# Performance work log

Measured on AMD Instinct MI355X. Metric: run time of the kernel, lower is better.

## Reference

```python
import jax, jax.numpy as jnp
import numpy as np


def conv1d_same(x, w, b, dilation=1):
    # x: [B, T, Cin], w: [K, Cin, Cout] (WIO), 'same' padding, stride 1
    y = jax.lax.conv_general_dilated(
        x, w, window_strides=(1,), padding='SAME',
        rhs_dilation=(dilation,), dimension_numbers=('NWC', 'WIO', 'NWC'))
    return y + b


def setup_inputs() -> dict:
    key = jax.random.key(0)
    ks = jax.random.split(key, 6)
    B, T, N_IN, N_OUT, ATTN_DIM, KSZ = 16, 2048, 96, 128, 64, 3
    return {
        'x': jax.random.normal(ks[0], (B, T, N_IN), jnp.float32),
        'qkv_w': jax.random.normal(ks[1], (N_IN, 3 * ATTN_DIM), jnp.float32) * 0.05,
        'qkv_b': jnp.zeros((3 * ATTN_DIM,), jnp.float32),
        'scale': jnp.ones((), jnp.float32),
        'conv_w1': jax.random.normal(ks[2], (KSZ, ATTN_DIM, N_OUT), jnp.float32) * 0.05,
        'conv_b1': jnp.zeros((N_OUT,), jnp.float32),
        'conv_w2': jax.random.normal(ks[3], (KSZ, N_OUT, N_OUT), jnp.float32) * 0.05,
        'conv_b2': jnp.zeros((N_OUT,), jnp.float32),
        'down_w': jax.random.normal(ks[4], (N_IN, N_OUT), jnp.float32) * 0.1,
    }


def reference(x, qkv_w, qkv_b, scale, conv_w1, conv_b1, conv_w2, conv_b2, down_w):
    # Dense4Attention: single Dense(3*attn_dim), split into q,k,v
    qkv = x @ qkv_w + qkv_b                       # [B,T,3*D]
    q, k, v = jnp.split(qkv, 3, axis=-1)          # each [B,T,D]
    # AttentionBlock: scores = q k^T * learned scale; non-causal (default)
    scores = jnp.einsum('btd,bsd->bts', q, k) * scale   # [B,T,T]
    weights = jax.nn.softmax(scores, axis=2)            # softmax_axis=2
    out_attn = jnp.einsum('bts,bsd->btd', weights, v)   # [B,T,D]
    h = jax.nn.relu(conv1d_same(out_attn, conv_w1, conv_b1, 1))
    out = jax.nn.relu(conv1d_same(h, conv_w2, conv_b2, 1))   # [B,T,n_out]
    # enhanced residual: softmax over time of row-sums of attn weights
    weight_x = jax.nn.softmax(jnp.sum(weights, axis=2), axis=1)  # [B,T]
    en_res_x = (weight_x[..., None] * x) @ down_w   # n_in != n_out -> downsample
    res = x @ down_w                                 # skip path downsample
    return jax.nn.relu(out + res + en_res_x)
```

## Files before the change

kernel.cpp:

```cpp
#include <hip/hip_runtime.h>
#include <cstdint>

#define B_   16
#define T_   2048
#define CIN  96
#define DH   64
#define NOUT 128

typedef float floatx4 __attribute__((ext_vector_type(4)));
typedef short shortx8 __attribute__((ext_vector_type(8)));

__device__ __forceinline__ unsigned short f2bf(float f) {
  unsigned int u = __float_as_uint(f);
  u += 0x7FFFu + ((u >> 16) & 1u);
  return (unsigned short)(u >> 16);
}
__device__ __forceinline__ floatx4 f4zero() { floatx4 v; v[0]=0.f;v[1]=0.f;v[2]=0.f;v[3]=0.f; return v; }
__device__ __forceinline__ shortx8 s8zero() { shortx8 v;
#pragma unroll
  for (int i=0;i<8;++i) v[i]=0; return v; }

__global__ __launch_bounds__(256) void k_wprep(
    const float* __restrict__ qkv_w, const float* __restrict__ cw1,
    const float* __restrict__ cw2, const float* __restrict__ dw,
    unsigned short* __restrict__ qwt, unsigned short* __restrict__ w1t,
    unsigned short* __restrict__ w2t, unsigned short* __restrict__ dwt)
{
  int o = blockIdx.x * 256 + threadIdx.x;
  if (o < 18432) {
    int co = o / 96, ci = o % 96;
    qwt[o] = f2bf(qkv_w[ci * 192 + co]);
  } else if (o < 43008) {
    int p = o - 18432;
    int tap = p / 8192, rem = p % 8192, co = rem >> 6, ci = rem & 63;
    w1t[p] = f2bf(cw1[(tap * 64 + ci) * 128 + co]);
  } else if (o < 92160) {
    int p = o - 43008;
    int tap = p / 16384, rem = p % 16384, co = rem >> 7, ci = rem & 127;
    w2t[p] = f2bf(cw2[(tap * 128 + ci) * 128 + co]);
  } else if (o < 104448) {
    int p = o - 92160;
    int co = p / 96, ci = p % 96;
    dwt[p] = f2bf(dw[ci * 128 + co]);
  }
}

__global__ __launch_bounds__(256) void k_qkv(
    const float* __restrict__ x, const unsigned short* __restrict__ qwt,
    const float* __restrict__ qkv_b, const float* __restrict__ scale_p,
    unsigned short* __restrict__ qb, unsigned short* __restrict__ kb,
    unsigned short* __restrict__ vT)
{
  __shared__ __align__(16) unsigned short Xs[64][104];
  const int bx = blockIdx.x;
  const int b = bx >> 5, t0 = (bx & 31) * 64;
  const int tid = threadIdx.x, wave = tid >> 6, lane = tid & 63;
  const int l15 = lane & 15, quad = lane >> 4;
  const float scl2 = scale_p[0] * 1.4426950408889634f;

  for (int idx = tid; idx < 64 * 24; idx += 256) {
    int r = idx / 24, c = (idx % 24) * 4;
    float4 xv = *(const float4*)(x + ((size_t)(b * T_ + t0 + r)) * CIN + c);
    ushort4 o; o.x = f2bf(xv.x); o.y = f2bf(xv.y); o.z = f2bf(xv.z); o.w = f2bf(xv.w);
    *(ushort4*)(&Xs[r][c]) = o;
  }
  __syncthreads();

  floatx4 acc[4][3];
#pragma unroll
  for (int mt = 0; mt < 4; ++mt)
#pragma unroll
    for (int nt = 0; nt < 3; ++nt) acc[mt][nt] = f4zero();

#pragma unroll
  for (int ks = 0; ks < 3; ++ks) {
    shortx8 wf[3];
#pragma unroll
    for (int nt = 0; nt < 3; ++nt) {
      int j = wave * 48 + nt * 16 + l15;
      wf[nt] = *(const shortx8*)(qwt + (size_t)j * 96 + ks * 32 + quad * 8);
    }
#pragma unroll
    for (int mt = 0; mt < 4; ++mt) {
      shortx8 af = *(const shortx8*)(&Xs[mt * 16 + l15][ks * 32 + quad * 8]);
#pragma unroll
      for (int nt = 0; nt < 3; ++nt)
        acc[mt][nt] = __builtin_amdgcn_mfma_f32_16x16x32_bf16(af, wf[nt], acc[mt][nt], 0, 0, 0);
    }
  }

#pragma unroll
  for (int nt = 0; nt < 3; ++nt) {
    int j0 = wave * 48 + nt * 16;
    int j = j0 + l15;
    float bias = qkv_b[j];
#pragma unroll
    for (int mt = 0; mt < 4; ++mt) {
#pragma unroll
      for (int r = 0; r < 4; ++r) {
        int t = t0 + mt * 16 + quad * 4 + r;
        float v = acc[mt][nt][r] + bias;
        if (j0 < 64)        qb[((size_t)b * T_ + t) * DH + j] = f2bf(v * scl2);
        else if (j0 < 128)  kb[((size_t)b * T_ + t) * DH + (j - 64)] = f2bf(v);
        else                vT[((size_t)b * DH + (j - 128)) * T_ + t] = f2bf(v);
      }
    }
  }
}

__global__ __launch_bounds__(256) void k_attn(
    const unsigned short* __restrict__ qb, const unsigned short* __restrict__ kb,
    const unsigned short* __restrict__ vT,
    float* __restrict__ opart, float* __restrict__ lws)
{
  __shared__ __align__(16) unsigned short Kt[64][72];
  __shared__ __align__(16) unsigned short Vt[80][72];
  __shared__ __align__(16) unsigned short Pt[4][16][72];
  const int bx = blockIdx.x;
  const int half = bx & 1, qt = (bx >> 1) & 31, b = bx >> 6;
  const int tid = threadIdx.x, wave = tid >> 6, lane = tid & 63;
  const int l15 = lane & 15, quad = lane >> 4;

  const unsigned short* qrow = qb + ((size_t)b * T_ + qt * 64 + wave * 16 + l15) * DH;
  shortx8 qf0 = *(const shortx8*)(qrow + quad * 8);
  shortx8 qf1 = *(const shortx8*)(qrow + 32 + quad * 8);

  floatx4 O[5];
#pragma unroll
  for (int i = 0; i < 5; ++i) O[i] = f4zero();

  const unsigned short* kbase = kb + (size_t)b * T_ * DH + (size_t)half * 1024 * DH;
  const unsigned short* vbase = vT + (size_t)b * DH * T_ + half * 1024;

  for (int idx = tid; idx < 16 * 72; idx += 256) {
    int r = idx / 72, c = idx % 72;
    Vt[64 + r][c] = (r == 0) ? (unsigned short)0x3F80 : (unsigned short)0;
  }

  const int kr0 = tid >> 3, kc = (tid & 7) * 8;
  shortx8 pk[2], pv[2];
#pragma unroll
  for (int i = 0; i < 2; ++i) {
    pk[i] = *(const shortx8*)(kbase + (size_t)(kr0 + i * 32) * DH + kc);
    pv[i] = *(const shortx8*)(vbase + (size_t)(kr0 + i * 32) * T_ + kc);
  }

  for (int t = 0; t < 16; ++t) {
#pragma unroll
    for (int i = 0; i < 2; ++i) {
      *(shortx8*)(&Kt[kr0 + i * 32][kc]) = pk[i];
      *(shortx8*)(&Vt[kr0 + i * 32][kc]) = pv[i];
    }
    __syncthreads();

    if (t < 15) {
      int s0 = (t + 1) * 64;
#pragma unroll
      for (int i = 0; i < 2; ++i) {
        pk[i] = *(const shortx8*)(kbase + (size_t)(s0 + kr0 + i * 32) * DH + kc);
        pv[i] = *(const shortx8*)(vbase + (size_t)(kr0 + i * 32) * T_ + s0 + kc);
      }
    }

    floatx4 S[4];
#pragma unroll
    for (int nt = 0; nt < 4; ++nt) {
      S[nt] = f4zero();
      shortx8 bk0 = *(const shortx8*)(&Kt[nt * 16 + l15][quad * 8]);
      shortx8 bk1 = *(const shortx8*)(&Kt[nt * 16 + l15][32 + quad * 8]);
      S[nt] = __builtin_amdgcn_mfma_f32_16x16x32_bf16(qf0, bk0, S[nt], 0, 0, 0);
      S[nt] = __builtin_amdgcn_mfma_f32_16x16x32_bf16(qf1, bk1, S[nt], 0, 0, 0);
    }

#pragma unroll
    for (int r = 0; r < 4; ++r)
#pragma unroll
      for (int nt = 0; nt < 4; ++nt) {
        float p = exp2f(S[nt][r]);
        Pt[wave][quad * 4 + r][(nt * 16 + l15 + (quad << 4)) & 63] = f2bf(p);
      }

#pragma unroll
    for (int kk = 0; kk < 2; ++kk) {
      int pcol = (kk * 32 + quad * 8 + ((l15 >> 2) << 4)) & 63;
      shortx8 ap = *(const shortx8*)(&Pt[wave][l15][pcol]);
#pragma unroll
      for (int dt = 0; dt < 5; ++dt) {
        shortx8 bv = *(const shortx8*)(&Vt[dt * 16 + l15][kk * 32 + quad * 8]);
        O[dt] = __builtin_amdgcn_mfma_f32_16x16x32_bf16(ap, bv, O[dt], 0, 0, 0);
      }
    }
    __syncthreads();
  }

  float* obase = opart + (((size_t)(half * B_ + b) * T_) + qt * 64 + wave * 16) * DH;
#pragma unroll
  for (int r = 0; r < 4; ++r) {
    int row = quad * 4 + r;
#pragma unroll
    for (int dt = 0; dt < 4; ++dt)
      obase[(size_t)row * DH + dt * 16 + l15] = O[dt][r];
    if (l15 == 0)
      lws[half * (B_ * T_) + b * T_ + qt * 64 + wave * 16 + row] = O[4][r];
  }
}

__global__ __launch_bounds__(256) void k_comb(
    const float* __restrict__ opart, const float* __restrict__ lws,
    unsigned short* __restrict__ ab)
{
  int g = blockIdx.x * 256 + threadIdx.x;
  int bt = g >> 4, dg = (g & 15) * 4;
  const size_t HS = (size_t)B_ * T_ * DH;
  float4 p0 = *(const float4*)(opart + (size_t)bt * DH + dg);
  float4 p1 = *(const float4*)(opart + HS + (size_t)bt * DH + dg);
  float inv = 1.f / (lws[bt] + lws[B_ * T_ + bt]);
  ushort4 o;
  o.x = f2bf((p0.x + p1.x) * inv);
  o.y = f2bf((p0.y + p1.y) * inv);
  o.z = f2bf((p0.z + p1.z) * inv);
  o.w = f2bf((p0.w + p1.w) * inv);
  *(ushort4*)(ab + (size_t)bt * DH + dg) = o;
}

__global__ __launch_bounds__(256) void k_conv1(
    const unsigned short* __restrict__ ab, const unsigned short* __restrict__ w1t,
    const float* __restrict__ b1, unsigned short* __restrict__ hb)
{
  __shared__ __align__(16) unsigned short At[66][72];
  const int bx = blockIdx.x;
  const int b = bx >> 5, t0 = (bx & 31) * 64;
  const int tid = threadIdx.x, wave = tid >> 6, lane = tid & 63;
  const int l15 = lane & 15, quad = lane >> 4;

  for (int idx = tid; idx < 66 * 8; idx += 256) {
    int r = idx >> 3, c = (idx & 7) * 8;
    int t = t0 + r - 1;
    shortx8 v = s8zero();
    if (t >= 0 && t < T_) v = *(const shortx8*)(ab + ((size_t)b * T_ + t) * DH + c);
    *(shortx8*)(&At[r][c]) = v;
  }
  __syncthreads();

  floatx4 acc[4][2];
#pragma unroll
  for (int mt = 0; mt < 4; ++mt) { acc[mt][0] = f4zero(); acc[mt][1] = f4zero(); }

#pragma unroll
  for (int tap = 0; tap < 3; ++tap) {
#pragma unroll
    for (int ks = 0; ks < 2; ++ks) {
      shortx8 wf[2];
#pragma unroll
      for (int ct = 0; ct < 2; ++ct) {
        int co = wave * 32 + ct * 16 + l15;
        wf[ct] = *(const shortx8*)(w1t + ((size_t)tap * 128 + co) * 64 + ks * 32 + quad * 8);
      }
#pragma unroll
      for (int mt = 0; mt < 4; ++mt) {
        shortx8 af = *(const shortx8*)(&At[mt * 16 + l15 + tap][ks * 32 + quad * 8]);
        acc[mt][0] = __builtin_amdgcn_mfma_f32_16x16x32_bf16(af, wf[0], acc[mt][0], 0, 0, 0);
        acc[mt][1] = __builtin_amdgcn_mfma_f32_16x16x32_bf16(af, wf[1], acc[mt][1], 0, 0, 0);
      }
    }
  }

#pragma unroll
  for (int ct = 0; ct < 2; ++ct) {
    int co = wave * 32 + ct * 16 + l15;
    float bias = b1[co];
#pragma unroll
    for (int mt = 0; mt < 4; ++mt)
#pragma unroll
      for (int r = 0; r < 4; ++r) {
        int t = t0 + mt * 16 + quad * 4 + r;
        hb[((size_t)b * T_ + t) * NOUT + co] = f2bf(fmaxf(acc[mt][ct][r] + bias, 0.f));
      }
  }
}

__global__ __launch_bounds__(256) void k_conv2(
    const unsigned short* __restrict__ hb, const float* __restrict__ x,
    const unsigned short* __restrict__ w2t, const unsigned short* __restrict__ dwt,
    const float* __restrict__ b2, float* __restrict__ out)
{
  __shared__ __align__(16) unsigned short Ht[66][136];
  __shared__ __align__(16) unsigned short Xt[64][104];
  const int bx = blockIdx.x;
  const int b = bx >> 5, t0 = (bx & 31) * 64;
  const int tid = threadIdx.x, wave = tid >> 6, lane = tid & 63;
  const int l15 = lane & 15, quad = lane >> 4;

  for (int idx = tid; idx < 66 * 16; idx += 256) {
    int r = idx >> 4, c = (idx & 15) * 8;
    int t = t0 + r - 1;
    shortx8 v = s8zero();
    if (t >= 0 && t < T_) v = *(const shortx8*)(hb + ((size_t)b * T_ + t) * NOUT + c);
    *(shortx8*)(&Ht[r][c]) = v;
  }
  for (int idx = tid; idx < 64 * 24; idx += 256) {
    int r = idx / 24, c = (idx % 24) * 4;
    float4 xv = *(const float4*)(x + ((size_t)(b * T_ + t0 + r)) * CIN + c);
    ushort4 o; o.x = f2bf(xv.x); o.y = f2bf(xv.y); o.z = f2bf(xv.z); o.w = f2bf(xv.w);
    *(ushort4*)(&Xt[r][c]) = o;
  }
  __syncthreads();

  floatx4 a2[4][2], ar[4][2];
#pragma unroll
  for (int mt = 0; mt < 4; ++mt) { a2[mt][0]=f4zero(); a2[mt][1]=f4zero(); ar[mt][0]=f4zero(); ar[mt][1]=f4zero(); }

#pragma unroll
  for (int tap = 0; tap < 3; ++tap) {
#pragma unroll
    for (int ks = 0; ks < 4; ++ks) {
      shortx8 wf[2];
#pragma unroll
      for (int ct = 0; ct < 2; ++ct) {
        int co = wave * 32 + ct * 16 + l15;
        wf[ct] = *(const shortx8*)(w2t + ((size_t)tap * 128 + co) * 128 + ks * 32 + quad * 8);
      }
#pragma unroll
      for (int mt = 0; mt < 4; ++mt) {
        shortx8 af = *(const shortx8*)(&Ht[mt * 16 + l15 + tap][ks * 32 + quad * 8]);
        a2[mt][0] = __builtin_amdgcn_mfma_f32_16x16x32_bf16(af, wf[0], a2[mt][0], 0, 0, 0);
        a2[mt][1] = __builtin_amdgcn_mfma_f32_16x16x32_bf16(af, wf[1], a2[mt][1], 0, 0, 0);
      }
    }
  }
#pragma unroll
  for (int ks = 0; ks < 3; ++ks) {
    shortx8 wf[2];
#pragma unroll
    for (int ct = 0; ct < 2; ++ct) {
      int co = wave * 32 + ct * 16 + l15;
      wf[ct] = *(const shortx8*)(dwt + (size_t)co * 96 + ks * 32 + quad * 8);
    }
#pragma unroll
    for (int mt = 0; mt < 4; ++mt) {
      shortx8 af = *(const shortx8*)(&Xt[mt * 16 + l15][ks * 32 + quad * 8]);
      ar[mt][0] = __builtin_amdgcn_mfma_f32_16x16x32_bf16(af, wf[0], ar[mt][0], 0, 0, 0);
      ar[mt][1] = __builtin_amdgcn_mfma_f32_16x16x32_bf16(af, wf[1], ar[mt][1], 0, 0, 0);
    }
  }

  const float kres = 1.0f + 1.0f / 2048.0f;
#pragma unroll
  for (int ct = 0; ct < 2; ++ct) {
    int co = wave * 32 + ct * 16 + l15;
    float bias = b2[co];
#pragma unroll
    for (int mt = 0; mt < 4; ++mt)
#pragma unroll
      for (int r = 0; r < 4; ++r) {
        int t = t0 + mt * 16 + quad * 4 + r;
        float o2 = fmaxf(a2[mt][ct][r] + bias, 0.f);
        out[((size_t)b * T_ + t) * NOUT + co] = fmaxf(o2 + ar[mt][ct][r] * kres, 0.f);
      }
  }
}

extern "C" void kernel_launch(void* const* d_in, const int* in_sizes, int n_in,
                              void* d_out, int out_size, void* d_ws, size_t ws_size,
                              hipStream_t stream) {
  const float* x      = (const float*)d_in[0];
  const float* qkv_w  = (const float*)d_in[1];
  const float* qkv_b  = (const float*)d_in[2];
  const float* scale  = (const float*)d_in[3];
  const float* cw1    = (const float*)d_in[4];
  const float* cb1    = (const float*)d_in[5];
  const float* cw2    = (const float*)d_in[6];
  const float* cb2    = (const float*)d_in[7];
  const float* dw     = (const float*)d_in[8];

  char* ws = (char*)d_ws;
  unsigned short* qb  = (unsigned short*)(ws + 0);
  unsigned short* kb  = (unsigned short*)(ws + 4194304);
  unsigned short* vT  = (unsigned short*)(ws + 8388608);
  unsigned short* ab  = (unsigned short*)(ws + 12582912);
  unsigned short* hb  = (unsigned short*)(ws + 16777216);
  unsigned short* qwt = (unsigned short*)(ws + 25165824);
  unsigned short* w1t = (unsigned short*)(ws + 25202688);
  unsigned short* w2t = (unsigned short*)(ws + 25251840);
  unsigned short* dwt = (unsigned short*)(ws + 25350144);
  float*          lws = (float*)(ws + 25374720);

  float* opart = (float*)d_out;

  k_wprep<<<408, 256, 0, stream>>>(qkv_w, cw1, cw2, dw, qwt, w1t, w2t, dwt);
  k_qkv  <<<512, 256, 0, stream>>>(x, qwt, qkv_b, scale, qb, kb, vT);
  k_attn <<<1024, 256, 0, stream>>>(qb, kb, vT, opart, lws);
  k_comb <<<2048, 256, 0, stream>>>(opart, lws, ab);
  k_conv1<<<512, 256, 0, stream>>>(ab, w1t, cb1, hb);
  k_conv2<<<512, 256, 0, stream>>>(hb, x, w2t, dwt, cb2, (float*)d_out);
}
```

Baseline: 155.0 us.

## Split attention four ways, fuse combine into conv1, halve tiles, bf16 partials

The attention kernel now splits keys into four chunks instead of two and keeps V fragments in registers loaded straight from global memory, so the V tile in shared memory goes away. The row-sum comes from an MFMA against a constant ones vector, and the P tile is written with vector stores in a transposed layout. Partial outputs are stored as bf16, and the separate combine kernel is folded into conv1's load stage. The qkv, conv1 and conv2 tiles shrink from 64 to 32 rows, doubling the grid size. The V stores are vectorised as well. In exchange, partials lose precision and each V fragment is loaded from global memory with a strided access pattern.

```diff
diff --git a/kernel.cpp b/kernel.cpp
--- a/kernel.cpp
+++ b/kernel.cpp
@@ -9,11 +9,15 @@
 
 typedef float floatx4 __attribute__((ext_vector_type(4)));
 typedef short shortx8 __attribute__((ext_vector_type(8)));
+typedef unsigned short ushortx4 __attribute__((ext_vector_type(4)));
 
 __device__ __forceinline__ unsigned short f2bf(float f) {
   unsigned int u = __float_as_uint(f);
   u += 0x7FFFu + ((u >> 16) & 1u);
   return (unsigned short)(u >> 16);
+}
+__device__ __forceinline__ float bf2f(unsigned short u) {
+  return __uint_as_float(((unsigned int)u) << 16);
 }
 __device__ __forceinline__ floatx4 f4zero() { floatx4 v; v[0]=0.f;v[1]=0.f;v[2]=0.f;v[3]=0.f; return v; }
 __device__ __forceinline__ shortx8 s8zero() { shortx8 v;
@@ -51,14 +55,14 @@
     unsigned short* __restrict__ qb, unsigned short* __restrict__ kb,
     unsigned short* __restrict__ vT)
 {
-  __shared__ __align__(16) unsigned short Xs[64][104];
+  __shared__ __align__(16) unsigned short Xs[32][104];
   const int bx = blockIdx.x;
-  const int b = bx >> 5, t0 = (bx & 31) * 64;
+  const int b = bx >> 6, t0 = (bx & 63) * 32;
   const int tid = threadIdx.x, wave = tid >> 6, lane = tid & 63;
   const int l15 = lane & 15, quad = lane >> 4;
   const float scl2 = scale_p[0] * 1.4426950408889634f;
 
-  for (int idx = tid; idx < 64 * 24; idx += 256) {
+  for (int idx = tid; idx < 32 * 24; idx += 256) {
     int r = idx / 24, c = (idx % 24) * 4;
     float4 xv = *(const float4*)(x + ((size_t)(b * T_ + t0 + r)) * CIN + c);
     ushort4 o; o.x = f2bf(xv.x); o.y = f2bf(xv.y); o.z = f2bf(xv.z); o.w = f2bf(xv.w);
@@ -66,9 +70,9 @@
   }
   __syncthreads();
 
-  floatx4 acc[4][3];
-#pragma unroll
-  for (int mt = 0; mt < 4; ++mt)
+  floatx4 acc[2][3];
+#pragma unroll
+  for (int mt = 0; mt < 2; ++mt)
 #pragma unroll
     for (int nt = 0; nt < 3; ++nt) acc[mt][nt] = f4zero();
 
@@ -81,7 +85,7 @@
       wf[nt] = *(const shortx8*)(qwt + (size_t)j * 96 + ks * 32 + quad * 8);
     }
 #pragma unroll
-    for (int mt = 0; mt < 4; ++mt) {
+    for (int mt = 0; mt < 2; ++mt) {
       shortx8 af = *(const shortx8*)(&Xs[mt * 16 + l15][ks * 32 + quad * 8]);
 #pragma unroll
       for (int nt = 0; nt < 3; ++nt)
@@ -94,30 +98,40 @@
     int j0 = wave * 48 + nt * 16;
     int j = j0 + l15;
     float bias = qkv_b[j];
-#pragma unroll
-    for (int mt = 0; mt < 4; ++mt) {
-#pragma unroll
-      for (int r = 0; r < 4; ++r) {
-        int t = t0 + mt * 16 + quad * 4 + r;
-        float v = acc[mt][nt][r] + bias;
-        if (j0 < 64)        qb[((size_t)b * T_ + t) * DH + j] = f2bf(v * scl2);
-        else if (j0 < 128)  kb[((size_t)b * T_ + t) * DH + (j - 64)] = f2bf(v);
-        else                vT[((size_t)b * DH + (j - 128)) * T_ + t] = f2bf(v);
-      }
-    }
-  }
-}
-
-__global__ __launch_bounds__(256) void k_attn(
+    if (j0 < 128) {
+#pragma unroll
+      for (int mt = 0; mt < 2; ++mt)
+#pragma unroll
+        for (int r = 0; r < 4; ++r) {
+          int t = t0 + mt * 16 + quad * 4 + r;
+          float v = acc[mt][nt][r] + bias;
+          if (j0 < 64) qb[((size_t)b * T_ + t) * DH + j] = f2bf(v * scl2);
+          else         kb[((size_t)b * T_ + t) * DH + (j - 64)] = f2bf(v);
+        }
+    } else {
+      int d = j - 128;
+#pragma unroll
+      for (int mt = 0; mt < 2; ++mt) {
+        ushortx4 u;
+        u[0] = f2bf(acc[mt][nt][0] + bias);
+        u[1] = f2bf(acc[mt][nt][1] + bias);
+        u[2] = f2bf(acc[mt][nt][2] + bias);
+        u[3] = f2bf(acc[mt][nt][3] + bias);
+        *(ushortx4*)(vT + ((size_t)b * DH + d) * T_ + t0 + mt * 16 + quad * 4) = u;
+      }
+    }
+  }
+}
+
+__global__ __launch_bounds__(256, 4) void k_attn(
     const unsigned short* __restrict__ qb, const unsigned short* __restrict__ kb,
     const unsigned short* __restrict__ vT,
-    float* __restrict__ opart, float* __restrict__ lws)
+    unsigned short* __restrict__ opart, float* __restrict__ lws)
 {
   __shared__ __align__(16) unsigned short Kt[64][72];
-  __shared__ __align__(16) unsigned short Vt[80][72];
   __shared__ __align__(16) unsigned short Pt[4][16][72];
   const int bx = blockIdx.x;
-  const int half = bx & 1, qt = (bx >> 1) & 31, b = bx >> 6;
+  const int half = bx & 3, qt = (bx >> 2) & 31, b = bx >> 7;
   const int tid = threadIdx.x, wave = tid >> 6, lane = tid & 63;
   const int l15 = lane & 15, quad = lane >> 4;
 
@@ -129,122 +143,117 @@
 #pragma unroll
   for (int i = 0; i < 5; ++i) O[i] = f4zero();
 
-  const unsigned short* kbase = kb + (size_t)b * T_ * DH + (size_t)half * 1024 * DH;
-  const unsigned short* vbase = vT + (size_t)b * DH * T_ + half * 1024;
-
-  for (int idx = tid; idx < 16 * 72; idx += 256) {
-    int r = idx / 72, c = idx % 72;
-    Vt[64 + r][c] = (r == 0) ? (unsigned short)0x3F80 : (unsigned short)0;
-  }
+  shortx8 ones;
+#pragma unroll
+  for (int i = 0; i < 8; ++i) ones[i] = (short)0x3F80;
+
+  const unsigned short* kbase = kb + (size_t)b * T_ * DH + (size_t)half * 512 * DH;
+  const unsigned short* vbase = vT + (size_t)b * DH * T_ + half * 512;
 
   const int kr0 = tid >> 3, kc = (tid & 7) * 8;
-  shortx8 pk[2], pv[2];
-#pragma unroll
-  for (int i = 0; i < 2; ++i) {
-    pk[i] = *(const shortx8*)(kbase + (size_t)(kr0 + i * 32) * DH + kc);
-    pv[i] = *(const shortx8*)(vbase + (size_t)(kr0 + i * 32) * T_ + kc);
-  }
-
-  for (int t = 0; t < 16; ++t) {
-#pragma unroll
-    for (int i = 0; i < 2; ++i) {
-      *(shortx8*)(&Kt[kr0 + i * 32][kc]) = pk[i];
-      *(shortx8*)(&Vt[kr0 + i * 32][kc]) = pv[i];
-    }
+  shortx8 pk[2];
+  pk[0] = *(const shortx8*)(kbase + (size_t)kr0 * DH + kc);
+  pk[1] = *(const shortx8*)(kbase + (size_t)(kr0 + 32) * DH + kc);
+
+  for (int t = 0; t < 8; ++t) {
+    *(shortx8*)(&Kt[kr0][kc]) = pk[0];
+    *(shortx8*)(&Kt[kr0 + 32][kc]) = pk[1];
     __syncthreads();
-
-    if (t < 15) {
-      int s0 = (t + 1) * 64;
-#pragma unroll
-      for (int i = 0; i < 2; ++i) {
-        pk[i] = *(const shortx8*)(kbase + (size_t)(s0 + kr0 + i * 32) * DH + kc);
-        pv[i] = *(const shortx8*)(vbase + (size_t)(kr0 + i * 32) * T_ + s0 + kc);
-      }
+    const int s0 = t * 64;
+
+    shortx8 bv[2][4];
+#pragma unroll
+    for (int kk = 0; kk < 2; ++kk)
+#pragma unroll
+      for (int dt = 0; dt < 4; ++dt)
+        bv[kk][dt] = *(const shortx8*)(vbase + (size_t)(dt * 16 + l15) * T_ + s0 + kk * 32 + quad * 8);
+
+    if (t < 7) {
+      pk[0] = *(const shortx8*)(kbase + (size_t)(s0 + 64 + kr0) * DH + kc);
+      pk[1] = *(const shortx8*)(kbase + (size_t)(s0 + 64 + kr0 + 32) * DH + kc);
     }
 
     floatx4 S[4];
 #pragma unroll
     for (int nt = 0; nt < 4; ++nt) {
-      S[nt] = f4zero();
       shortx8 bk0 = *(const shortx8*)(&Kt[nt * 16 + l15][quad * 8]);
       shortx8 bk1 = *(const shortx8*)(&Kt[nt * 16 + l15][32 + quad * 8]);
-      S[nt] = __builtin_amdgcn_mfma_f32_16x16x32_bf16(qf0, bk0, S[nt], 0, 0, 0);
-      S[nt] = __builtin_amdgcn_mfma_f32_16x16x32_bf16(qf1, bk1, S[nt], 0, 0, 0);
-    }
-
-#pragma unroll
-    for (int r = 0; r < 4; ++r)
-#pragma unroll
-      for (int nt = 0; nt < 4; ++nt) {
-        float p = exp2f(S[nt][r]);
-        Pt[wave][quad * 4 + r][(nt * 16 + l15 + (quad << 4)) & 63] = f2bf(p);
-      }
+      S[nt] = __builtin_amdgcn_mfma_f32_16x16x32_bf16(bk0, qf0, f4zero(), 0, 0, 0);
+      S[nt] = __builtin_amdgcn_mfma_f32_16x16x32_bf16(bk1, qf1, S[nt], 0, 0, 0);
+    }
+
+#pragma unroll
+    for (int nt = 0; nt < 4; ++nt) {
+      ushortx4 u;
+      u[0] = f2bf(exp2f(S[nt][0]));
+      u[1] = f2bf(exp2f(S[nt][1]));
+      u[2] = f2bf(exp2f(S[nt][2]));
+      u[3] = f2bf(exp2f(S[nt][3]));
+      *(ushortx4*)(&Pt[wave][l15][nt * 16 + quad * 4]) = u;
+    }
+    asm volatile("" ::: "memory");
 
 #pragma unroll
     for (int kk = 0; kk < 2; ++kk) {
-      int pcol = (kk * 32 + quad * 8 + ((l15 >> 2) << 4)) & 63;
-      shortx8 ap = *(const shortx8*)(&Pt[wave][l15][pcol]);
-#pragma unroll
-      for (int dt = 0; dt < 5; ++dt) {
-        shortx8 bv = *(const shortx8*)(&Vt[dt * 16 + l15][kk * 32 + quad * 8]);
-        O[dt] = __builtin_amdgcn_mfma_f32_16x16x32_bf16(ap, bv, O[dt], 0, 0, 0);
-      }
+      shortx8 ap = *(const shortx8*)(&Pt[wave][l15][kk * 32 + quad * 8]);
+#pragma unroll
+      for (int dt = 0; dt < 4; ++dt)
+        O[dt] = __builtin_amdgcn_mfma_f32_16x16x32_bf16(ap, bv[kk][dt], O[dt], 0, 0, 0);
+      O[4] = __builtin_amdgcn_mfma_f32_16x16x32_bf16(ap, ones, O[4], 0, 0, 0);
     }
     __syncthreads();
   }
 
-  float* obase = opart + (((size_t)(half * B_ + b) * T_) + qt * 64 + wave * 16) * DH;
+  unsigned short* obase = opart + (((size_t)(half * B_ + b) * T_) + qt * 64 + wave * 16) * DH;
 #pragma unroll
   for (int r = 0; r < 4; ++r) {
     int row = quad * 4 + r;
 #pragma unroll
     for (int dt = 0; dt < 4; ++dt)
-      obase[(size_t)row * DH + dt * 16 + l15] = O[dt][r];
+      obase[(size_t)row * DH + dt * 16 + l15] = f2bf(O[dt][r]);
     if (l15 == 0)
-      lws[half * (B_ * T_) + b * T_ + qt * 64 + wave * 16 + row] = O[4][r];
-  }
-}
-
-__global__ __launch_bounds__(256) void k_comb(
-    const float* __restrict__ opart, const float* __restrict__ lws,
-    unsigned short* __restrict__ ab)
+      lws[(half * B_ + b) * T_ + qt * 64 + wave * 16 + row] = O[4][r];
+  }
+}
+
+__global__ __launch_bounds__(256) void k_conv1(
+    const unsigned short* __restrict__ opart, const float* __restrict__ lws,
+    const unsigned short* __restrict__ w1t, const float* __restrict__ b1,
+    unsigned short* __restrict__ hb)
 {
-  int g = blockIdx.x * 256 + threadIdx.x;
-  int bt = g >> 4, dg = (g & 15) * 4;
-  const size_t HS = (size_t)B_ * T_ * DH;
-  float4 p0 = *(const float4*)(opart + (size_t)bt * DH + dg);
-  float4 p1 = *(const float4*)(opart + HS + (size_t)bt * DH + dg);
-  float inv = 1.f / (lws[bt] + lws[B_ * T_ + bt]);
-  ushort4 o;
-  o.x = f2bf((p0.x + p1.x) * inv);
-  o.y = f2bf((p0.y + p1.y) * inv);
-  o.z = f2bf((p0.z + p1.z) * inv);
-  o.w = f2bf((p0.w + p1.w) * inv);
-  *(ushort4*)(ab + (size_t)bt * DH + dg) = o;
-}
-
-__global__ __launch_bounds__(256) void k_conv1(
-    const unsigned short* __restrict__ ab, const unsigned short* __restrict__ w1t,
-    const float* __restrict__ b1, unsigned short* __restrict__ hb)
-{
-  __shared__ __align__(16) unsigned short At[66][72];
+  __shared__ __align__(16) unsigned short At[34][72];
   const int bx = blockIdx.x;
-  const int b = bx >> 5, t0 = (bx & 31) * 64;
+  const int b = bx >> 6, t0 = (bx & 63) * 32;
   const int tid = threadIdx.x, wave = tid >> 6, lane = tid & 63;
   const int l15 = lane & 15, quad = lane >> 4;
 
-  for (int idx = tid; idx < 66 * 8; idx += 256) {
+  for (int idx = tid; idx < 34 * 8; idx += 256) {
     int r = idx >> 3, c = (idx & 7) * 8;
     int t = t0 + r - 1;
     shortx8 v = s8zero();
-    if (t >= 0 && t < T_) v = *(const shortx8*)(ab + ((size_t)b * T_ + t) * DH + c);
+    if (t >= 0 && t < T_) {
+      float a8[8];
+#pragma unroll
+      for (int e = 0; e < 8; ++e) a8[e] = 0.f;
+      float lsum = 0.f;
+#pragma unroll
+      for (int s = 0; s < 4; ++s) {
+        shortx8 u = *(const shortx8*)(opart + (((size_t)(s * B_ + b)) * T_ + t) * DH + c);
+#pragma unroll
+        for (int e = 0; e < 8; ++e) a8[e] += bf2f((unsigned short)u[e]);
+        lsum += lws[(s * B_ + b) * T_ + t];
+      }
+      float inv = 1.f / lsum;
+#pragma unroll
+      for (int e = 0; e < 8; ++e) v[e] = (short)f2bf(a8[e] * inv);
+    }
     *(shortx8*)(&At[r][c]) = v;
   }
   __syncthreads();
 
-  floatx4 acc[4][2];
-#pragma unroll
-  for (int mt = 0; mt < 4; ++mt) { acc[mt][0] = f4zero(); acc[mt][1] = f4zero(); }
+  floatx4 acc[2][2];
+#pragma unroll
+  for (int mt = 0; mt < 2; ++mt) { acc[mt][0] = f4zero(); acc[mt][1] = f4zero(); }
 
 #pragma unroll
   for (int tap = 0; tap < 3; ++tap) {
@@ -257,7 +266,7 @@
         wf[ct] = *(const shortx8*)(w1t + ((size_t)tap * 128 + co) * 64 + ks * 32 + quad * 8);
       }
 #pragma unroll
-      for (int mt = 0; mt < 4; ++mt) {
+      for (int mt = 0; mt < 2; ++mt) {
         shortx8 af = *(const shortx8*)(&At[mt * 16 + l15 + tap][ks * 32 + quad * 8]);
         acc[mt][0] = __builtin_amdgcn_mfma_f32_16x16x32_bf16(af, wf[0], acc[mt][0], 0, 0, 0);
         acc[mt][1] = __builtin_amdgcn_mfma_f32_16x16x32_bf16(af, wf[1], acc[mt][1], 0, 0, 0);
@@ -270,7 +279,7 @@
     int co = wave * 32 + ct * 16 + l15;
     float bias = b1[co];
 #pragma unroll
-    for (int mt = 0; mt < 4; ++mt)
+    for (int mt = 0; mt < 2; ++mt)
 #pragma unroll
       for (int r = 0; r < 4; ++r) {
         int t = t0 + mt * 16 + quad * 4 + r;
@@ -284,21 +293,21 @@
     const unsigned short* __restrict__ w2t, const unsigned short* __restrict__ dwt,
     const float* __restrict__ b2, float* __restrict__ out)
 {
-  __shared__ __align__(16) unsigned short Ht[66][136];
-  __shared__ __align__(16) unsigned short Xt[64][104];
+  __shared__ __align__(16) unsigned short Ht[34][136];
+  __shared__ __align__(16) unsigned short Xt[32][104];
   const int bx = blockIdx.x;
-  const int b = bx >> 5, t0 = (bx & 31) * 64;
+  const int b = bx >> 6, t0 = (bx & 63) * 32;
   const int tid = threadIdx.x, wave = tid >> 6, lane = tid & 63;
   const int l15 = lane & 15, quad = lane >> 4;
 
-  for (int idx = tid; idx < 66 * 16; idx += 256) {
+  for (int idx = tid; idx < 34 * 16; idx += 256) {
     int r = idx >> 4, c = (idx & 15) * 8;
     int t = t0 + r - 1;
     shortx8 v = s8zero();
     if (t >= 0 && t < T_) v = *(const shortx8*)(hb + ((size_t)b * T_ + t) * NOUT + c);
     *(shortx8*)(&Ht[r][c]) = v;
   }
-  for (int idx = tid; idx < 64 * 24; idx += 256) {
+  for (int idx = tid; idx < 32 * 24; idx += 256) {
     int r = idx / 24, c = (idx % 24) * 4;
     float4 xv = *(const float4*)(x + ((size_t)(b * T_ + t0 + r)) * CIN + c);
     ushort4 o; o.x = f2bf(xv.x); o.y = f2bf(xv.y); o.z = f2bf(xv.z); o.w = f2bf(xv.w);
@@ -306,9 +315,9 @@
   }
   __syncthreads();
 
-  floatx4 a2[4][2], ar[4][2];
-#pragma unroll
-  for (int mt = 0; mt < 4; ++mt) { a2[mt][0]=f4zero(); a2[mt][1]=f4zero(); ar[mt][0]=f4zero(); ar[mt][1]=f4zero(); }
+  floatx4 a2[2][2], ar[2][2];
+#pragma unroll
+  for (int mt = 0; mt < 2; ++mt) { a2[mt][0]=f4zero(); a2[mt][1]=f4zero(); ar[mt][0]=f4zero(); ar[mt][1]=f4zero(); }
 
 #pragma unroll
   for (int tap = 0; tap < 3; ++tap) {
@@ -321,7 +330,7 @@
         wf[ct] = *(const shortx8*)(w2t + ((size_t)tap * 128 + co) * 128 + ks * 32 + quad * 8);
       }
 #pragma unroll
-      for (int mt = 0; mt < 4; ++mt) {
+      for (int mt = 0; mt < 2; ++mt) {
         shortx8 af = *(const shortx8*)(&Ht[mt * 16 + l15 + tap][ks * 32 + quad * 8]);
         a2[mt][0] = __builtin_amdgcn_mfma_f32_16x16x32_bf16(af, wf[0], a2[mt][0], 0, 0, 0);
         a2[mt][1] = __builtin_amdgcn_mfma_f32_16x16x32_bf16(af, wf[1], a2[mt][1], 0, 0, 0);
@@ -337,7 +346,7 @@
       wf[ct] = *(const shortx8*)(dwt + (size_t)co * 96 + ks * 32 + quad * 8);
     }
 #pragma unroll
-    for (int mt = 0; mt < 4; ++mt) {
+    for (int mt = 0; mt < 2; ++mt) {
       shortx8 af = *(const shortx8*)(&Xt[mt * 16 + l15][ks * 32 + quad * 8]);
       ar[mt][0] = __builtin_amdgcn_mfma_f32_16x16x32_bf16(af, wf[0], ar[mt][0], 0, 0, 0);
       ar[mt][1] = __builtin_amdgcn_mfma_f32_16x16x32_bf16(af, wf[1], ar[mt][1], 0, 0, 0);
@@ -350,7 +359,7 @@
     int co = wave * 32 + ct * 16 + l15;
     float bias = b2[co];
 #pragma unroll
-    for (int mt = 0; mt < 4; ++mt)
+    for (int mt = 0; mt < 2; ++mt)
 #pragma unroll
       for (int r = 0; r < 4; ++r) {
         int t = t0 + mt * 16 + quad * 4 + r;
@@ -377,20 +386,18 @@
   unsigned short* qb  = (unsigned short*)(ws + 0);
   unsigned short* kb  = (unsigned short*)(ws + 4194304);
   unsigned short* vT  = (unsigned short*)(ws + 8388608);
-  unsigned short* ab  = (unsigned short*)(ws + 12582912);
-  unsigned short* hb  = (unsigned short*)(ws + 16777216);
-  unsigned short* qwt = (unsigned short*)(ws + 25165824);
-  unsigned short* w1t = (unsigned short*)(ws + 25202688);
-  unsigned short* w2t = (unsigned short*)(ws + 25251840);
-  unsigned short* dwt = (unsigned short*)(ws + 25350144);
-  float*          lws = (float*)(ws + 25374720);
-
-  float* opart = (float*)d_out;
+  unsigned short* hb  = (unsigned short*)(ws + 12582912);
+  unsigned short* qwt = (unsigned short*)(ws + 20971520);
+  unsigned short* w1t = (unsigned short*)(ws + 21008384);
+  unsigned short* w2t = (unsigned short*)(ws + 21057536);
+  unsigned short* dwt = (unsigned short*)(ws + 21155840);
+  float*          lws = (float*)(ws + 21180416);
+
+  unsigned short* opart = (unsigned short*)d_out;
 
   k_wprep<<<408, 256, 0, stream>>>(qkv_w, cw1, cw2, dw, qwt, w1t, w2t, dwt);
-  k_qkv  <<<512, 256, 0, stream>>>(x, qwt, qkv_b, scale, qb, kb, vT);
-  k_attn <<<1024, 256, 0, stream>>>(qb, kb, vT, opart, lws);
-  k_comb <<<2048, 256, 0, stream>>>(opart, lws, ab);
-  k_conv1<<<512, 256, 0, stream>>>(ab, w1t, cb1, hb);
-  k_conv2<<<512, 256, 0, stream>>>(hb, x, w2t, dwt, cb2, (float*)d_out);
-}
+  k_qkv  <<<1024, 256, 0, stream>>>(x, qwt, qkv_b, scale, qb, kb, vT);
+  k_attn <<<2048, 256, 0, stream>>>(qb, kb, vT, opart, lws);
+  k_conv1<<<1024, 256, 0, stream>>>(opart, lws, w1t, cb1, hb);
+  k_conv2<<<1024, 256, 0, stream>>>(hb, x, w2t, dwt, cb2, (float*)d_out);
+}
```

Measured after the change: 187.1 us. 1.21x slower.
